# Kernel tuning notes

Hardware: AMD Instinct MI355X
Metric: run time of the kernel (lower is better)

The kernel has to match this reference:

```python
import jax, jax.numpy as jnp
import numpy as np

STEPS = 3


def setup_inputs() -> dict:
    key = jax.random.key(0)
    ks = jax.random.split(key, 6)
    N, H, B = 1000000, 128, 16384
    x = jax.random.normal(ks[0], (N, H), dtype=jnp.float32)
    batch_vec = jnp.sort(jax.random.randint(ks[1], (N,), 0, B)).astype(jnp.int64)
    scale_ih = 1.0 / np.sqrt(2 * H)
    scale_hh = 1.0 / np.sqrt(H)
    W_ih = jax.random.normal(ks[2], (4 * H, 2 * H), dtype=jnp.float32) * scale_ih
    W_hh = jax.random.normal(ks[3], (4 * H, H), dtype=jnp.float32) * scale_hh
    b_ih = jnp.zeros((4 * H,), dtype=jnp.float32)
    b_hh = jnp.zeros((4 * H,), dtype=jnp.float32)
    return {"x": x, "batch_vec": batch_vec, "W_ih": W_ih, "W_hh": W_hh,
            "b_ih": b_ih, "b_hh": b_hh, "num_graphs": B}


def _set2set(x, batch_vec, W_ih, W_hh, b_ih, b_hh, B):
    N, H = x.shape
    q_star = jnp.zeros((B, 2 * H), x.dtype)
    h = jnp.zeros((B, H), x.dtype)
    c = jnp.zeros((B, H), x.dtype)
    bias = b_ih + b_hh
    for _ in range(STEPS):
        # LSTMCell (torch gate order: i, f, g, o)
        gates = q_star @ W_ih.T + h @ W_hh.T + bias  # [B, 4H]
        i, f, g, o = jnp.split(gates, 4, axis=-1)
        c = jax.nn.sigmoid(f) * c + jax.nn.sigmoid(i) * jnp.tanh(g)
        h = jax.nn.sigmoid(o) * jnp.tanh(c)
        q = h  # [B, H]
        # attention logits per node
        e = jnp.sum(x * q[batch_vec], axis=-1)  # [N]
        emax = jax.ops.segment_max(e, batch_vec, num_segments=B)
        emax = jax.lax.stop_gradient(jnp.where(jnp.isfinite(emax), emax, 0.0))
        ex = jnp.exp(e - emax[batch_vec])
        denom = jax.ops.segment_sum(ex, batch_vec, num_segments=B)
        a = ex / denom[batch_vec]  # segment softmax, [N]
        r = jax.ops.segment_sum(a[:, None] * x, batch_vec, num_segments=B)  # [B, H]
        q_star = jnp.concatenate([q, r], axis=-1)  # [B, 2H]
    return q_star


def reference(x, batch_vec, W_ih, W_hh, b_ih, b_hh, num_graphs):
    return _set2set(x, batch_vec, W_ih, W_hh, b_ih, b_hh, int(num_graphs))
```

## Files before the change

kernel.cpp:

```cpp
#include <hip/hip_runtime.h>
#include <math.h>

#define HDIM 128
#define G4 512
#define TS 36

typedef float vf4 __attribute__((ext_vector_type(4)));

__device__ __forceinline__ float sigm(float v) { return 1.0f / (1.0f + __expf(-v)); }
__device__ __forceinline__ float ftanh(float v) {
    return 1.0f - 2.0f / (__expf(2.0f * v) + 1.0f);
}
__device__ __forceinline__ float dot4(vf4 a, vf4 b) {
    return a.x * b.x + a.y * b.y + a.z * b.z + a.w * b.w;
}

__global__ __launch_bounds__(256) void k_setup(const float* __restrict__ W_ih,
                                               const float* __restrict__ W_hh,
                                               const float* __restrict__ b_ih,
                                               const float* __restrict__ b_hh,
                                               const int* __restrict__ batch_vec, int N, int B,
                                               float* __restrict__ Wc, int* __restrict__ seg_start,
                                               float* __restrict__ h, float* __restrict__ c) {
    int t = blockIdx.x * 256 + threadIdx.x;
    if (t < B * HDIM) {
        int hid = t & (HDIM - 1);
        float gi = b_ih[hid] + b_hh[hid];
        float gg = b_ih[2 * HDIM + hid] + b_hh[2 * HDIM + hid];
        float go = b_ih[3 * HDIM + hid] + b_hh[3 * HDIM + hid];
        float cv = sigm(gi) * ftanh(gg);
        c[t] = cv;
        h[t] = sigm(go) * ftanh(cv);
    }
    if (t < G4 * 2 * HDIM) {
        int g = t >> 8;
        int k = t & 255;
        float w = W_ih[g * 256 + k];
        if (k < HDIM) w += W_hh[g * HDIM + k];
        Wc[t] = w;
    }
    if (t <= B) {
        int lo = 0, hi = N;
        while (lo < hi) {
            int mid = (lo + hi) >> 1;
            if (batch_vec[mid] < t) lo = mid + 1; else hi = mid;
        }
        seg_start[t] = lo;
    }
}

#define UPD(m_, d_, ra_, rb_, p_, xa_, xb_)  \
    {                                        \
        float mn_ = fmaxf(m_, p_);           \
        float sc_ = __expf(m_ - mn_);        \
        float pe_ = __expf(p_ - mn_);        \
        d_ = d_ * sc_ + pe_;                 \
        ra_ = ra_ * sc_ + pe_ * xa_;         \
        rb_ = rb_ * sc_ + pe_ * xb_;         \
        m_ = mn_;                            \
    }

__global__ __launch_bounds__(256) void k_attn(const float* __restrict__ x,
                                              const float* __restrict__ q,
                                              const int* __restrict__ seg_start,
                                              float* __restrict__ r_out, int ldr, int col_off,
                                              int B, int rev) {
    int wave = threadIdx.x >> 6;
    int lane = threadIdx.x & 63;
    int l16 = lane & 15;
    int quarter = lane >> 4;
    int gid = (blockIdx.x << 2) + wave;
    if (gid >= B) return;
    int seg = rev ? (B - 1 - gid) : gid;
    int s = seg_start[seg];
    int e = seg_start[seg + 1];

    const float* qrow = q + (size_t)seg * HDIM;
    vf4 qa = *(const vf4*)(qrow + l16 * 4);
    vf4 qb = *(const vf4*)(qrow + 64 + l16 * 4);

    float m0 = 0.0f, d0 = 0.0f, m1 = 0.0f, d1 = 0.0f;
    vf4 ra0 = {0.f, 0.f, 0.f, 0.f}, rb0 = {0.f, 0.f, 0.f, 0.f};
    vf4 ra1 = {0.f, 0.f, 0.f, 0.f}, rb1 = {0.f, 0.f, 0.f, 0.f};

    int base = s;
#pragma unroll 2
    for (; base + 8 <= e; base += 8) {
        const float* xr0 = x + (size_t)(base + quarter) * HDIM;
        const float* xr1 = xr0 + 4 * HDIM;
        vf4 xa0 = *(const vf4*)(xr0 + l16 * 4), xb0 = *(const vf4*)(xr0 + 64 + l16 * 4);
        vf4 xa1 = *(const vf4*)(xr1 + l16 * 4), xb1 = *(const vf4*)(xr1 + 64 + l16 * 4);
        float p0 = dot4(xa0, qa) + dot4(xb0, qb);
        float p1 = dot4(xa1, qa) + dot4(xb1, qb);
        p0 += __shfl_xor(p0, 1, 64);  p1 += __shfl_xor(p1, 1, 64);
        p0 += __shfl_xor(p0, 2, 64);  p1 += __shfl_xor(p1, 2, 64);
        p0 += __shfl_xor(p0, 4, 64);  p1 += __shfl_xor(p1, 4, 64);
        p0 += __shfl_xor(p0, 8, 64);  p1 += __shfl_xor(p1, 8, 64);
        UPD(m0, d0, ra0, rb0, p0, xa0, xb0)
        UPD(m1, d1, ra1, rb1, p1, xa1, xb1)
    }
    for (; base < e; base += 4) {
        int row = base + quarter;
        const float* xr = x + (size_t)min(row, e - 1) * HDIM;
        vf4 xa = *(const vf4*)(xr + l16 * 4), xb = *(const vf4*)(xr + 64 + l16 * 4);
        float p = dot4(xa, qa) + dot4(xb, qb);
        p += __shfl_xor(p, 1, 64);
        p += __shfl_xor(p, 2, 64);
        p += __shfl_xor(p, 4, 64);
        p += __shfl_xor(p, 8, 64);
        if (row >= e) p = -1e30f;
        UPD(m0, d0, ra0, rb0, p, xa, xb)
    }
    {
        float M = fmaxf(m0, m1);
        float w0 = __expf(m0 - M), w1 = __expf(m1 - M);
        d0 = d0 * w0 + d1 * w1;
        ra0 = ra0 * w0 + ra1 * w1;
        rb0 = rb0 * w0 + rb1 * w1;
        m0 = M;
    }
#pragma unroll
    for (int off = 16; off <= 32; off <<= 1) {
        float om = __shfl_xor(m0, off, 64);
        float M = fmaxf(m0, om);
        float w = __expf(m0 - M);
        d0 *= w;
        ra0 *= w;
        rb0 *= w;
        d0 += __shfl_xor(d0, off, 64);
        ra0.x += __shfl_xor(ra0.x, off, 64);
        ra0.y += __shfl_xor(ra0.y, off, 64);
        ra0.z += __shfl_xor(ra0.z, off, 64);
        ra0.w += __shfl_xor(ra0.w, off, 64);
        rb0.x += __shfl_xor(rb0.x, off, 64);
        rb0.y += __shfl_xor(rb0.y, off, 64);
        rb0.z += __shfl_xor(rb0.z, off, 64);
        rb0.w += __shfl_xor(rb0.w, off, 64);
        m0 = M;
    }
    float inv = (d0 > 0.0f) ? 1.0f / d0 : 0.0f;
    float* dst = r_out + (size_t)seg * ldr + col_off;
    if (quarter == 0) {
        vf4 o = ra0 * inv;
        *(vf4*)(dst + l16 * 4) = o;
    } else if (quarter == 1) {
        vf4 o = rb0 * inv;
        *(vf4*)(dst + 64 + l16 * 4) = o;
    }
}

__global__ __launch_bounds__(256) void k_gemm_lstm(const float* __restrict__ h_prev,
                                                   const float* __restrict__ r_prev,
                                                   const float* __restrict__ c_prev,
                                                   const float* __restrict__ Wc,
                                                   const float* __restrict__ b_ih,
                                                   const float* __restrict__ b_hh,
                                                   float* __restrict__ h_new,
                                                   float* __restrict__ c_new,
                                                   float* __restrict__ h_mirror) {
    __shared__ float As[128 * TS];
    __shared__ float Ws[64 * TS];
    int ct = blockIdx.y;
    int rb = blockIdx.x * 128;
    int tid = threadIdx.x;
    int tx = tid & 15, ty = tid >> 4;
    float acc[8][4];
#pragma unroll
    for (int i = 0; i < 8; ++i)
#pragma unroll
        for (int j = 0; j < 4; ++j) acc[i][j] = 0.0f;

    for (int kc = 0; kc < 8; ++kc) {
        const float* src = (kc < 4) ? h_prev : r_prev;
        int kbase = (kc & 3) * 32;
#pragma unroll
        for (int i = 0; i < 4; ++i) {
            int li = tid + i * 256;
            int row = li >> 3;
            int c4 = (li & 7) * 4;
            *(vf4*)&As[row * TS + c4] = *(const vf4*)(src + (size_t)(rb + row) * HDIM + kbase + c4);
        }
#pragma unroll
        for (int i = 0; i < 2; ++i) {
            int li = tid + i * 256;
            int col = li >> 3;
            int c4 = (li & 7) * 4;
            int g = ct * 16 + (col & 15) + 128 * (col >> 4);
            *(vf4*)&Ws[col * TS + c4] = *(const vf4*)(Wc + (size_t)g * 256 + kc * 32 + c4);
        }
        __syncthreads();
#pragma unroll
        for (int k = 0; k < 32; k += 4) {
            vf4 a[8], b[4];
#pragma unroll
            for (int i = 0; i < 8; ++i) a[i] = *(vf4*)&As[(ty + 16 * i) * TS + k];
#pragma unroll
            for (int j = 0; j < 4; ++j) b[j] = *(vf4*)&Ws[(tx + 16 * j) * TS + k];
#pragma unroll
            for (int i = 0; i < 8; ++i)
#pragma unroll
                for (int j = 0; j < 4; ++j) {
                    acc[i][j] += a[i].x * b[j].x + a[i].y * b[j].y +
                                 a[i].z * b[j].z + a[i].w * b[j].w;
                }
        }
        __syncthreads();
    }
    int hidx = ct * 16 + tx;
    float bi = b_ih[hidx] + b_hh[hidx];
    float bf = b_ih[HDIM + hidx] + b_hh[HDIM + hidx];
    float bg = b_ih[2 * HDIM + hidx] + b_hh[2 * HDIM + hidx];
    float bo = b_ih[3 * HDIM + hidx] + b_hh[3 * HDIM + hidx];
#pragma unroll
    for (int i = 0; i < 8; ++i) {
        int row = rb + ty + 16 * i;
        float gi = acc[i][0] + bi;
        float gf = acc[i][1] + bf;
        float gg = acc[i][2] + bg;
        float go = acc[i][3] + bo;
        float cp = c_prev[(size_t)row * HDIM + hidx];
        float cn = sigm(gf) * cp + sigm(gi) * ftanh(gg);
        float hn = sigm(go) * ftanh(cn);
        c_new[(size_t)row * HDIM + hidx] = cn;
        h_new[(size_t)row * HDIM + hidx] = hn;
        if (h_mirror) h_mirror[(size_t)row * 2 * HDIM + hidx] = hn;
    }
}

extern "C" void kernel_launch(void* const* d_in, const int* in_sizes, int n_in,
                              void* d_out, int out_size, void* d_ws, size_t ws_size,
                              hipStream_t stream) {
    const float* x = (const float*)d_in[0];
    const int* batch_vec = (const int*)d_in[1];
    const float* W_ih = (const float*)d_in[2];
    const float* W_hh = (const float*)d_in[3];
    const float* b_ih = (const float*)d_in[4];
    const float* b_hh = (const float*)d_in[5];
    float* out = (float*)d_out;

    int N = in_sizes[1];
    int B = out_size / (2 * HDIM);

    char* ws = (char*)d_ws;
    float* Wc = (float*)ws;   ws += (size_t)G4 * 2 * HDIM * 4;
    float* h_a = (float*)ws;  ws += (size_t)B * HDIM * 4;
    float* h_b = (float*)ws;  ws += (size_t)B * HDIM * 4;
    float* cbuf = (float*)ws; ws += (size_t)B * HDIM * 4;
    float* rbuf = (float*)ws; ws += (size_t)B * HDIM * 4;
    int* seg = (int*)ws;      ws += (size_t)(B + 1) * 4;

    int setup_grid = (B * HDIM + 255) / 256;
    k_setup<<<setup_grid, 256, 0, stream>>>(W_ih, W_hh, b_ih, b_hh, batch_vec, N, B,
                                            Wc, seg, h_a, cbuf);

    dim3 ggrid(B / 128, 8);
    k_attn<<<(B + 3) / 4, 256, 0, stream>>>(x, h_a, seg, rbuf, HDIM, 0, B, 0);
    k_gemm_lstm<<<ggrid, 256, 0, stream>>>(h_a, rbuf, cbuf, Wc, b_ih, b_hh, h_b, cbuf, nullptr);
    k_attn<<<(B + 3) / 4, 256, 0, stream>>>(x, h_b, seg, rbuf, HDIM, 0, B, 1);
    k_gemm_lstm<<<ggrid, 256, 0, stream>>>(h_b, rbuf, cbuf, Wc, b_ih, b_hh, h_a, cbuf, out);
    k_attn<<<(B + 3) / 4, 256, 0, stream>>>(x, h_a, seg, out, 2 * HDIM, HDIM, B, 0);
}
```

Before: 559.3 us.

## Convert x to bf16 in first attention pass and reuse it in later passes

The first attention kernel now reads x in fp32 with nontemporal loads and also writes a bf16 copy to workspace. The second and third attention passes read that bf16 copy, halving the x bytes they pull from memory. Each lane now covers 8 contiguous columns instead of two 4-float chunks, and a single quarter writes the output. The cost is an extra 256MB write in the first pass and reduced precision of x in later steps, which changes numerics against the fp32 reference.

```diff
diff --git a/kernel.cpp b/kernel.cpp
--- a/kernel.cpp
+++ b/kernel.cpp
@@ -6,6 +6,7 @@
 #define TS 36
 
 typedef float vf4 __attribute__((ext_vector_type(4)));
+typedef unsigned short u16x8 __attribute__((ext_vector_type(8)));
 
 __device__ __forceinline__ float sigm(float v) { return 1.0f / (1.0f + __expf(-v)); }
 __device__ __forceinline__ float ftanh(float v) {
@@ -13,6 +14,17 @@
 }
 __device__ __forceinline__ float dot4(vf4 a, vf4 b) {
     return a.x * b.x + a.y * b.y + a.z * b.z + a.w * b.w;
+}
+__device__ __forceinline__ vf4 ldnt4(const float* p) {
+    return __builtin_nontemporal_load((const vf4*)p);
+}
+__device__ __forceinline__ unsigned short f2bf(float f) {
+    unsigned u = __float_as_uint(f);
+    u += 0x7fff + ((u >> 16) & 1);
+    return (unsigned short)(u >> 16);
+}
+__device__ __forceinline__ float bf2f(unsigned short h) {
+    return __uint_as_float(((unsigned)h) << 16);
 }
 
 __global__ __launch_bounds__(256) void k_setup(const float* __restrict__ W_ih,
@@ -60,24 +72,56 @@
         m_ = mn_;                            \
     }
 
-__global__ __launch_bounds__(256) void k_attn(const float* __restrict__ x,
-                                              const float* __restrict__ q,
-                                              const int* __restrict__ seg_start,
-                                              float* __restrict__ r_out, int ldr, int col_off,
-                                              int B, int rev) {
+#define MERGE_AND_WRITE()                                                     \
+    {                                                                         \
+        float M = fmaxf(m0, m1);                                              \
+        float w0 = __expf(m0 - M), w1 = __expf(m1 - M);                       \
+        d0 = d0 * w0 + d1 * w1;                                               \
+        ra0 = ra0 * w0 + ra1 * w1;                                            \
+        rb0 = rb0 * w0 + rb1 * w1;                                            \
+        m0 = M;                                                               \
+    }                                                                         \
+    _Pragma("unroll")                                                         \
+    for (int off = 16; off <= 32; off <<= 1) {                                \
+        float om = __shfl_xor(m0, off, 64);                                   \
+        float M = fmaxf(m0, om);                                              \
+        float w = __expf(m0 - M);                                             \
+        d0 *= w; ra0 *= w; rb0 *= w;                                          \
+        d0 += __shfl_xor(d0, off, 64);                                        \
+        ra0.x += __shfl_xor(ra0.x, off, 64);                                  \
+        ra0.y += __shfl_xor(ra0.y, off, 64);                                  \
+        ra0.z += __shfl_xor(ra0.z, off, 64);                                  \
+        ra0.w += __shfl_xor(ra0.w, off, 64);                                  \
+        rb0.x += __shfl_xor(rb0.x, off, 64);                                  \
+        rb0.y += __shfl_xor(rb0.y, off, 64);                                  \
+        rb0.z += __shfl_xor(rb0.z, off, 64);                                  \
+        rb0.w += __shfl_xor(rb0.w, off, 64);                                  \
+        m0 = M;                                                               \
+    }                                                                         \
+    float inv = (d0 > 0.0f) ? 1.0f / d0 : 0.0f;                               \
+    if (quarter == 0) {                                                       \
+        float* dst = r_out + (size_t)seg * ldr + col_off + l16 * 8;           \
+        *(vf4*)dst = ra0 * inv;                                               \
+        *(vf4*)(dst + 4) = rb0 * inv;                                         \
+    }
+
+__global__ __launch_bounds__(256) void k_attn_cvt(const float* __restrict__ x,
+                                                  unsigned short* __restrict__ x16,
+                                                  const float* __restrict__ q,
+                                                  const int* __restrict__ seg_start,
+                                                  float* __restrict__ r_out, int B) {
+    const int ldr = HDIM, col_off = 0;
     int wave = threadIdx.x >> 6;
     int lane = threadIdx.x & 63;
     int l16 = lane & 15;
     int quarter = lane >> 4;
-    int gid = (blockIdx.x << 2) + wave;
-    if (gid >= B) return;
-    int seg = rev ? (B - 1 - gid) : gid;
-    int s = seg_start[seg];
-    int e = seg_start[seg + 1];
-
-    const float* qrow = q + (size_t)seg * HDIM;
-    vf4 qa = *(const vf4*)(qrow + l16 * 4);
-    vf4 qb = *(const vf4*)(qrow + 64 + l16 * 4);
+    int seg = (blockIdx.x << 2) + wave;
+    if (seg >= B) return;
+    int s = seg_start[seg], e = seg_start[seg + 1];
+
+    const float* qrow = q + (size_t)seg * HDIM + l16 * 8;
+    vf4 qa = *(const vf4*)qrow;
+    vf4 qb = *(const vf4*)(qrow + 4);
 
     float m0 = 0.0f, d0 = 0.0f, m1 = 0.0f, d1 = 0.0f;
     vf4 ra0 = {0.f, 0.f, 0.f, 0.f}, rb0 = {0.f, 0.f, 0.f, 0.f};
@@ -86,10 +130,17 @@
     int base = s;
 #pragma unroll 2
     for (; base + 8 <= e; base += 8) {
-        const float* xr0 = x + (size_t)(base + quarter) * HDIM;
+        const float* xr0 = x + (size_t)(base + quarter) * HDIM + l16 * 8;
         const float* xr1 = xr0 + 4 * HDIM;
-        vf4 xa0 = *(const vf4*)(xr0 + l16 * 4), xb0 = *(const vf4*)(xr0 + 64 + l16 * 4);
-        vf4 xa1 = *(const vf4*)(xr1 + l16 * 4), xb1 = *(const vf4*)(xr1 + 64 + l16 * 4);
+        vf4 xa0 = ldnt4(xr0), xb0 = ldnt4(xr0 + 4);
+        vf4 xa1 = ldnt4(xr1), xb1 = ldnt4(xr1 + 4);
+        u16x8 c0, c1;
+        c0[0] = f2bf(xa0.x); c0[1] = f2bf(xa0.y); c0[2] = f2bf(xa0.z); c0[3] = f2bf(xa0.w);
+        c0[4] = f2bf(xb0.x); c0[5] = f2bf(xb0.y); c0[6] = f2bf(xb0.z); c0[7] = f2bf(xb0.w);
+        c1[0] = f2bf(xa1.x); c1[1] = f2bf(xa1.y); c1[2] = f2bf(xa1.z); c1[3] = f2bf(xa1.w);
+        c1[4] = f2bf(xb1.x); c1[5] = f2bf(xb1.y); c1[6] = f2bf(xb1.z); c1[7] = f2bf(xb1.w);
+        *(u16x8*)(x16 + (size_t)(base + quarter) * HDIM + l16 * 8) = c0;
+        *(u16x8*)(x16 + (size_t)(base + 4 + quarter) * HDIM + l16 * 8) = c1;
         float p0 = dot4(xa0, qa) + dot4(xb0, qb);
         float p1 = dot4(xa1, qa) + dot4(xb1, qb);
         p0 += __shfl_xor(p0, 1, 64);  p1 += __shfl_xor(p1, 1, 64);
@@ -101,8 +152,12 @@
     }
     for (; base < e; base += 4) {
         int row = base + quarter;
-        const float* xr = x + (size_t)min(row, e - 1) * HDIM;
-        vf4 xa = *(const vf4*)(xr + l16 * 4), xb = *(const vf4*)(xr + 64 + l16 * 4);
+        const float* xr = x + (size_t)min(row, e - 1) * HDIM + l16 * 8;
+        vf4 xa = ldnt4(xr), xb = ldnt4(xr + 4);
+        u16x8 c0;
+        c0[0] = f2bf(xa.x); c0[1] = f2bf(xa.y); c0[2] = f2bf(xa.z); c0[3] = f2bf(xa.w);
+        c0[4] = f2bf(xb.x); c0[5] = f2bf(xb.y); c0[6] = f2bf(xb.z); c0[7] = f2bf(xb.w);
+        *(u16x8*)(x16 + (size_t)min(row, e - 1) * HDIM + l16 * 8) = c0;
         float p = dot4(xa, qa) + dot4(xb, qb);
         p += __shfl_xor(p, 1, 64);
         p += __shfl_xor(p, 2, 64);
@@ -111,42 +166,65 @@
         if (row >= e) p = -1e30f;
         UPD(m0, d0, ra0, rb0, p, xa, xb)
     }
-    {
-        float M = fmaxf(m0, m1);
-        float w0 = __expf(m0 - M), w1 = __expf(m1 - M);
-        d0 = d0 * w0 + d1 * w1;
-        ra0 = ra0 * w0 + ra1 * w1;
-        rb0 = rb0 * w0 + rb1 * w1;
-        m0 = M;
-    }
-#pragma unroll
-    for (int off = 16; off <= 32; off <<= 1) {
-        float om = __shfl_xor(m0, off, 64);
-        float M = fmaxf(m0, om);
-        float w = __expf(m0 - M);
-        d0 *= w;
-        ra0 *= w;
-        rb0 *= w;
-        d0 += __shfl_xor(d0, off, 64);
-        ra0.x += __shfl_xor(ra0.x, off, 64);
-        ra0.y += __shfl_xor(ra0.y, off, 64);
-        ra0.z += __shfl_xor(ra0.z, off, 64);
-        ra0.w += __shfl_xor(ra0.w, off, 64);
-        rb0.x += __shfl_xor(rb0.x, off, 64);
-        rb0.y += __shfl_xor(rb0.y, off, 64);
-        rb0.z += __shfl_xor(rb0.z, off, 64);
-        rb0.w += __shfl_xor(rb0.w, off, 64);
-        m0 = M;
-    }
-    float inv = (d0 > 0.0f) ? 1.0f / d0 : 0.0f;
-    float* dst = r_out + (size_t)seg * ldr + col_off;
-    if (quarter == 0) {
-        vf4 o = ra0 * inv;
-        *(vf4*)(dst + l16 * 4) = o;
-    } else if (quarter == 1) {
-        vf4 o = rb0 * inv;
-        *(vf4*)(dst + 64 + l16 * 4) = o;
-    }
+    MERGE_AND_WRITE()
+}
+
+__global__ __launch_bounds__(256) void k_attn_b16(const unsigned short* __restrict__ x16,
+                                                  const float* __restrict__ q,
+                                                  const int* __restrict__ seg_start,
+                                                  float* __restrict__ r_out, int ldr, int col_off,
+                                                  int B, int rev) {
+    int wave = threadIdx.x >> 6;
+    int lane = threadIdx.x & 63;
+    int l16 = lane & 15;
+    int quarter = lane >> 4;
+    int gid = (blockIdx.x << 2) + wave;
+    if (gid >= B) return;
+    int seg = rev ? (B - 1 - gid) : gid;
+    int s = seg_start[seg], e = seg_start[seg + 1];
+
+    const float* qrow = q + (size_t)seg * HDIM + l16 * 8;
+    vf4 qa = *(const vf4*)qrow;
+    vf4 qb = *(const vf4*)(qrow + 4);
+
+    float m0 = 0.0f, d0 = 0.0f, m1 = 0.0f, d1 = 0.0f;
+    vf4 ra0 = {0.f, 0.f, 0.f, 0.f}, rb0 = {0.f, 0.f, 0.f, 0.f};
+    vf4 ra1 = {0.f, 0.f, 0.f, 0.f}, rb1 = {0.f, 0.f, 0.f, 0.f};
+
+    int base = s;
+#pragma unroll 2
+    for (; base + 8 <= e; base += 8) {
+        const unsigned short* xr0 = x16 + (size_t)(base + quarter) * HDIM + l16 * 8;
+        u16x8 u0 = *(const u16x8*)xr0;
+        u16x8 u1 = *(const u16x8*)(xr0 + 4 * HDIM);
+        vf4 xa0 = {bf2f(u0[0]), bf2f(u0[1]), bf2f(u0[2]), bf2f(u0[3])};
+        vf4 xb0 = {bf2f(u0[4]), bf2f(u0[5]), bf2f(u0[6]), bf2f(u0[7])};
+        vf4 xa1 = {bf2f(u1[0]), bf2f(u1[1]), bf2f(u1[2]), bf2f(u1[3])};
+        vf4 xb1 = {bf2f(u1[4]), bf2f(u1[5]), bf2f(u1[6]), bf2f(u1[7])};
+        float p0 = dot4(xa0, qa) + dot4(xb0, qb);
+        float p1 = dot4(xa1, qa) + dot4(xb1, qb);
+        p0 += __shfl_xor(p0, 1, 64);  p1 += __shfl_xor(p1, 1, 64);
+        p0 += __shfl_xor(p0, 2, 64);  p1 += __shfl_xor(p1, 2, 64);
+        p0 += __shfl_xor(p0, 4, 64);  p1 += __shfl_xor(p1, 4, 64);
+        p0 += __shfl_xor(p0, 8, 64);  p1 += __shfl_xor(p1, 8, 64);
+        UPD(m0, d0, ra0, rb0, p0, xa0, xb0)
+        UPD(m1, d1, ra1, rb1, p1, xa1, xb1)
+    }
+    for (; base < e; base += 4) {
+        int row = base + quarter;
+        const unsigned short* xr = x16 + (size_t)min(row, e - 1) * HDIM + l16 * 8;
+        u16x8 u0 = *(const u16x8*)xr;
+        vf4 xa = {bf2f(u0[0]), bf2f(u0[1]), bf2f(u0[2]), bf2f(u0[3])};
+        vf4 xb = {bf2f(u0[4]), bf2f(u0[5]), bf2f(u0[6]), bf2f(u0[7])};
+        float p = dot4(xa, qa) + dot4(xb, qb);
+        p += __shfl_xor(p, 1, 64);
+        p += __shfl_xor(p, 2, 64);
+        p += __shfl_xor(p, 4, 64);
+        p += __shfl_xor(p, 8, 64);
+        if (row >= e) p = -1e30f;
+        UPD(m0, d0, ra0, rb0, p, xa, xb)
+    }
+    MERGE_AND_WRITE()
 }
 
 __global__ __launch_bounds__(256) void k_gemm_lstm(const float* __restrict__ h_prev,
@@ -242,21 +320,23 @@
     int B = out_size / (2 * HDIM);
 
     char* ws = (char*)d_ws;
-    float* Wc = (float*)ws;   ws += (size_t)G4 * 2 * HDIM * 4;
-    float* h_a = (float*)ws;  ws += (size_t)B * HDIM * 4;
-    float* h_b = (float*)ws;  ws += (size_t)B * HDIM * 4;
-    float* cbuf = (float*)ws; ws += (size_t)B * HDIM * 4;
-    float* rbuf = (float*)ws; ws += (size_t)B * HDIM * 4;
-    int* seg = (int*)ws;      ws += (size_t)(B + 1) * 4;
+    float* Wc = (float*)ws;            ws += (size_t)G4 * 2 * HDIM * 4;
+    float* h_a = (float*)ws;           ws += (size_t)B * HDIM * 4;
+    float* h_b = (float*)ws;           ws += (size_t)B * HDIM * 4;
+    float* cbuf = (float*)ws;          ws += (size_t)B * HDIM * 4;
+    float* rbuf = (float*)ws;          ws += (size_t)B * HDIM * 4;
+    int* seg = (int*)ws;               ws += (size_t)(B + 1) * 4;
+    ws = (char*)(((size_t)ws + 255) & ~(size_t)255);
+    unsigned short* x16 = (unsigned short*)ws;
 
     int setup_grid = (B * HDIM + 255) / 256;
     k_setup<<<setup_grid, 256, 0, stream>>>(W_ih, W_hh, b_ih, b_hh, batch_vec, N, B,
                                             Wc, seg, h_a, cbuf);
 
     dim3 ggrid(B / 128, 8);
-    k_attn<<<(B + 3) / 4, 256, 0, stream>>>(x, h_a, seg, rbuf, HDIM, 0, B, 0);
+    k_attn_cvt<<<(B + 3) / 4, 256, 0, stream>>>(x, x16, h_a, seg, rbuf, B);
     k_gemm_lstm<<<ggrid, 256, 0, stream>>>(h_a, rbuf, cbuf, Wc, b_ih, b_hh, h_b, cbuf, nullptr);
-    k_attn<<<(B + 3) / 4, 256, 0, stream>>>(x, h_b, seg, rbuf, HDIM, 0, B, 1);
+    k_attn_b16<<<(B + 3) / 4, 256, 0, stream>>>(x16, h_b, seg, rbuf, HDIM, 0, B, 1);
     k_gemm_lstm<<<ggrid, 256, 0, stream>>>(h_b, rbuf, cbuf, Wc, b_ih, b_hh, h_a, cbuf, out);
-    k_attn<<<(B + 3) / 4, 256, 0, stream>>>(x, h_a, seg, out, 2 * HDIM, HDIM, B, 0);
-}
+    k_attn_b16<<<(B + 3) / 4, 256, 0, stream>>>(x16, h_a, seg, out, 2 * HDIM, HDIM, B, 0);
+}
```

New measurement: 487.7 us. -12.8%, faster.
